# Optimization experiments

Measured on AMD Instinct MI355X. Metric: run time of the kernel, lower is better.

## Reference

```python
import jax, jax.numpy as jnp
import numpy as np

B, T, D = 4, 2048, 1024
H, DH = 16, 64

def setup_inputs() -> dict:
    key = jax.random.key(0)
    k1, k2, k3 = jax.random.split(key, 3)
    x = jax.random.normal(k1, (B, T, D), dtype=jnp.float32)
    ln_gamma = jnp.ones((D,), dtype=jnp.float32)
    ln_beta = jnp.zeros((D,), dtype=jnp.float32)
    W_qkv = jax.random.normal(k2, (3 * D, D), dtype=jnp.float32) * (1.0 / np.sqrt(D))
    W_o = jax.random.normal(k3, (D, D), dtype=jnp.float32) * (1.0 / np.sqrt(D))
    return {"x": x, "ln_gamma": ln_gamma, "ln_beta": ln_beta, "W_qkv": W_qkv, "W_o": W_o}

def reference(x, ln_gamma, ln_beta, W_qkv, W_o):
    b, t, d = x.shape
    scale = 1.0 / np.sqrt(DH)
    # pre-LN in fp32 (eps=1e-5, elementwise affine)
    xf = x.astype(jnp.float32)
    mu = jnp.mean(xf, axis=-1, keepdims=True)
    var = jnp.mean(jnp.square(xf - mu), axis=-1, keepdims=True)
    xn = (xf - mu) * jax.lax.rsqrt(var + 1e-5) * ln_gamma + ln_beta
    xn = xn.astype(x.dtype)
    # fused QKV projection (torch Linear: y = x @ W^T), view as (B,T,H,3*DH)
    qkv = jnp.einsum('btd,ed->bte', xn, W_qkv).reshape(b, t, H, 3 * DH)
    Q, K, V = jnp.split(qkv, 3, axis=-1)  # each (B,T,H,DH)
    # scores (B,H,T,T), causal mask, softmax
    scores = jnp.einsum('bqhd,bkhd->bhqk', Q, K) * scale
    causal = jnp.tril(jnp.ones((t, t), dtype=bool))
    scores = jnp.where(causal, scores, -jnp.inf)
    A = jax.nn.softmax(scores, axis=-1)
    ctx = jnp.einsum('bhqk,bkhd->bqhd', A, V).reshape(b, t, d)
    return jnp.einsum('btd,ed->bte', ctx, W_o)
```

## Files before the change

kernel.cpp:

```cpp
#include <hip/hip_runtime.h>


typedef __attribute__((ext_vector_type(8))) short bf8v;
typedef __attribute__((ext_vector_type(4))) float f4v;

#define Tt  2048
#define Dd  1024
#define Hh  16
#define DHh 64

#if __has_builtin(__builtin_amdgcn_exp2f)
#define EXP2(x) __builtin_amdgcn_exp2f(x)
#else
#define EXP2(x) __expf((x) * 0.69314718056f)
#endif

__device__ __forceinline__ ushort f2bf(float f) {
  union { float f; unsigned v; } c; c.f = f;
  unsigned r = c.v + 0x7fffu + ((c.v >> 16) & 1u);
  return (ushort)(r >> 16);
}
__device__ __forceinline__ ushort f2bf_rn(float f) {
  union { float f; unsigned v; } c; c.f = f;
  return (ushort)((c.v + 0x8000u) >> 16);
}
__device__ __forceinline__ f4v zero4() { f4v z; z[0]=z[1]=z[2]=z[3]=0.f; return z; }

__device__ __forceinline__ void gl_lds16(const ushort* g, ushort* l) {
  __builtin_amdgcn_global_load_lds(
      (const __attribute__((address_space(1))) unsigned*)g,
      (__attribute__((address_space(3))) unsigned*)l, 16, 0, 0);
}

__global__ __launch_bounds__(256)
void prep_k(const float* __restrict__ wqkv, ushort* __restrict__ wqkb,
            const float* __restrict__ wo,   ushort* __restrict__ wob,
            const float* __restrict__ x, const float* __restrict__ g,
            const float* __restrict__ bta, ushort* __restrict__ xn) {
  const int bid = blockIdx.x, tid = threadIdx.x;
  if (bid < 4096) {
    const float4* src = (bid < 3072) ? (const float4*)wqkv : (const float4*)wo;
    ushort4* dst      = (bid < 3072) ? (ushort4*)wqkb : (ushort4*)wob;
    const int i = ((bid < 3072) ? bid : (bid - 3072)) * 256 + tid;
    const float4 v = src[i];
    ushort4 o;
    o.x = f2bf(v.x); o.y = f2bf(v.y); o.z = f2bf(v.z); o.w = f2bf(v.w);
    dst[i] = o;
    return;
  }
  const int row = bid - 4096;
  const float4 v = ((const float4*)(x + row * Dd))[tid];
  float s  = v.x + v.y + v.z + v.w;
  float sq = v.x*v.x + v.y*v.y + v.z*v.z + v.w*v.w;
  #pragma unroll
  for (int off = 32; off; off >>= 1) {
    s  += __shfl_down(s,  off, 64);
    sq += __shfl_down(sq, off, 64);
  }
  __shared__ float red[8];
  const int w = tid >> 6, l = tid & 63;
  if (l == 0) { red[w] = s; red[w + 4] = sq; }
  __syncthreads();
  s  = red[0] + red[1] + red[2] + red[3];
  sq = red[4] + red[5] + red[6] + red[7];
  const float mu  = s * (1.0f / Dd);
  const float var = sq * (1.0f / Dd) - mu * mu;
  const float rs  = rsqrtf(var + 1e-5f);
  const float4 gv = ((const float4*)g)[tid];
  const float4 bv = ((const float4*)bta)[tid];
  ushort4 o;
  o.x = f2bf((v.x - mu) * rs * gv.x + bv.x);
  o.y = f2bf((v.y - mu) * rs * gv.y + bv.y);
  o.z = f2bf((v.z - mu) * rs * gv.z + bv.z);
  o.w = f2bf((v.w - mu) * rs * gv.w + bv.w);
  ((ushort4*)(xn + row * Dd))[tid] = o;
}

template<int MODE>
__global__ __launch_bounds__(256)
void gemm128(const ushort* __restrict__ A, const ushort* __restrict__ Bt,
             void* __restrict__ O0v, ushort* __restrict__ O1, ushort* __restrict__ O2,
             int Kd, int nbm) {
  __shared__ ushort As[2][128 * 64], Bs[2][128 * 64];
  const int tid = threadIdx.x;
  const int l = tid & 63, w = tid >> 6, fr = l & 15, fq = l >> 4;
  const int wm = w & 1, wn = w >> 1;
  const int bm = blockIdx.x % nbm, bn = blockIdx.x / nbm;
  const int gr8 = l >> 3, gc8s = ((l & 7) ^ gr8) * 8;
  const int sw = fr & 7;
  const int cA = (fq ^ sw) * 8, cB = ((4 + fq) ^ sw) * 8;
  const int NIT = Kd >> 6;

  f4v acc[4][4];
  #pragma unroll
  for (int m = 0; m < 4; m++)
    #pragma unroll
    for (int n = 0; n < 4; n++) acc[m][n] = zero4();

  auto stage = [&](int it, int bi) {
    const int k0 = it * 64;
    #pragma unroll
    for (int i = 0; i < 4; i++) {
      const int row = w * 32 + i * 8;
      gl_lds16(A  + (bm * 128 + row + gr8) * Kd + k0 + gc8s, &As[bi][row * 64]);
      gl_lds16(Bt + (bn * 128 + row + gr8) * Kd + k0 + gc8s, &Bs[bi][row * 64]);
    }
  };

  stage(0, 0);
  for (int it = 0; it < NIT; ++it) {
    __syncthreads();
    if (it + 1 < NIT) stage(it + 1, (it + 1) & 1);
    const ushort* Ab = As[it & 1];
    const ushort* Bb = Bs[it & 1];
    #pragma unroll
    for (int kk = 0; kk < 2; kk++) {
      const int cs = kk ? cB : cA;
      bf8v af[4], bf[4];
      #pragma unroll
      for (int m = 0; m < 4; m++)
        af[m] = *(const bf8v*)&Ab[(wm * 64 + m * 16 + fr) * 64 + cs];
      #pragma unroll
      for (int n = 0; n < 4; n++)
        bf[n] = *(const bf8v*)&Bb[(wn * 64 + n * 16 + fr) * 64 + cs];
      #pragma unroll
      for (int m = 0; m < 4; m++)
        #pragma unroll
        for (int n = 0; n < 4; n++)
          acc[m][n] = __builtin_amdgcn_mfma_f32_16x16x32_bf16(af[m], bf[n], acc[m][n], 0, 0, 0);
    }
  }

  #pragma unroll
  for (int m = 0; m < 4; m++) {
    const int grow = bm * 128 + wm * 64 + m * 16 + fq * 4;
    #pragma unroll
    for (int n = 0; n < 4; n++) {
      const int e = bn * 128 + wn * 64 + n * 16 + fr;
      #pragma unroll
      for (int r = 0; r < 4; r++) {
        const int row = grow + r;
        if (MODE == 0) {
          const int h = e / 192, inner = e % 192;
          const int sel = inner >> 6, dh = inner & 63;
          const int bb = row >> 11, t = row & 2047;
          float v = acc[m][n][r];
          if (sel == 0) v *= 0.18033688f;
          ushort* dst = (sel == 0) ? (ushort*)O0v : (sel == 1) ? O1 : O2;
          dst[((bb * Hh + h) * Tt + t) * DHh + dh] = f2bf(v);
        } else {
          ((float*)O0v)[row * Dd + e] = acc[m][n][r];
        }
      }
    }
  }
}

__global__ __launch_bounds__(256)
void vtr_k(const ushort* __restrict__ Vb, ushort* __restrict__ Vtg) {
  __shared__ ushort tile[64 * 72];
  const int tid = threadIdx.x;
  const int tt = blockIdx.x & 31;
  const int hb = blockIdx.x >> 5;
  const int base = hb * Tt * DHh;
  const int srow = tid >> 3, soff = (tid & 7) * 8;
  #pragma unroll
  for (int i = 0; i < 2; i++) {
    const int t = srow + i * 32;
    const uint4 vv = *(const uint4*)(Vb + base + (tt * 64 + t) * DHh + soff);
    const ushort* e = (const ushort*)&vv;
    #pragma unroll
    for (int j = 0; j < 8; j++) tile[(soff + j) * 72 + t] = e[j];
  }
  __syncthreads();
  #pragma unroll
  for (int i = 0; i < 2; i++) {
    const int dh = srow + i * 32;
    *(uint4*)(Vtg + base + dh * Tt + tt * 64 + soff) = *(const uint4*)&tile[dh * 72 + soff];
  }
}

__global__ __launch_bounds__(512)
void attn_k(const ushort* __restrict__ Qb, const ushort* __restrict__ Kb,
            const ushort* __restrict__ Vtg, ushort* __restrict__ ctx) {
  __shared__ ushort QS[128 * 64];
  __shared__ ushort Pb[128 * 68];
  __shared__ ushort Ks[2][64 * 64], Vt[2][64 * 64];
  const int tid = threadIdx.x;
  const int l = tid & 63, w = tid >> 6, fr = l & 15, fq = l >> 4;
  const int bid = blockIdx.x;
  const int hb = (bid & 7) * 8 + (bid >> 6);
  const int u  = (bid >> 3) & 7;
  const int h  = hb & 15, b = hb >> 4;
  const int headbase = hb * Tt * DHh;
  const int gr8 = l >> 3, gc8s = ((l & 7) ^ gr8) * 8;
  const int sw = fr & 7;
  const int cA = (fq ^ sw) * 8, cB = ((4 + fq) ^ sw) * 8;

  auto stageKV = [&](int kt, int bi) {
    const int row = w * 8;
    gl_lds16(Kb  + headbase + (kt * 64 + row + gr8) * DHh + gc8s, &Ks[bi][row * 64]);
    gl_lds16(Vtg + headbase + (row + gr8) * Tt + kt * 64 + gc8s, &Vt[bi][row * 64]);
  };

  for (int half = 0; half < 2; ++half) {
    const int qt = half ? (15 - u) : u;
    const int qrow0w = qt * 128 + w * 16;

    if (half) __syncthreads();

    #pragma unroll
    for (int i = 0; i < 2; i++) {
      const int row = w * 16 + i * 8;
      gl_lds16(Qb + headbase + (qt * 128 + row + gr8) * DHh + gc8s, &QS[row * 64]);
    }
    stageKV(0, 0);
    __syncthreads();

    bf8v aq[2];
    aq[0] = *(const bf8v*)&QS[(w * 16 + fr) * 64 + cA];
    aq[1] = *(const bf8v*)&QS[(w * 16 + fr) * 64 + cB];
    __asm__ __volatile__("" ::: "memory");

    f4v o[4];
    #pragma unroll
    for (int n = 0; n < 4; n++) o[n] = zero4();
    float lsum = 0.f;

    const int ktmax = 2 * qt + 1;
    for (int kt = 0; kt <= ktmax; ++kt) {
      if (kt) __syncthreads();
      if (kt < ktmax) stageKV(kt + 1, (kt + 1) & 1);
      const ushort* K_ = Ks[kt & 1];
      const ushort* V_ = Vt[kt & 1];

      if (kt * 64 <= qrow0w + 15) {
        f4v scT[4];
        #pragma unroll
        for (int n = 0; n < 4; n++) scT[n] = zero4();
        __builtin_amdgcn_s_setprio(1);
        #pragma unroll
        for (int nt = 0; nt < 4; nt++) {
          const bf8v k0 = *(const bf8v*)&K_[(nt * 16 + fr) * 64 + cA];
          const bf8v k1 = *(const bf8v*)&K_[(nt * 16 + fr) * 64 + cB];
          scT[nt] = __builtin_amdgcn_mfma_f32_16x16x32_bf16(k0, aq[0], scT[nt], 0, 0, 0);
          scT[nt] = __builtin_amdgcn_mfma_f32_16x16x32_bf16(k1, aq[1], scT[nt], 0, 0, 0);
        }
        __builtin_amdgcn_s_setprio(0);

        if (kt * 64 + 63 > qrow0w) {
          const int q0 = qrow0w + fr;
          #pragma unroll
          for (int nt = 0; nt < 4; nt++) {
            const int kc0 = kt * 64 + nt * 16 + fq * 4;
            #pragma unroll
            for (int r = 0; r < 4; r++)
              if (kc0 + r > q0) scT[nt][r] = -1e30f;
          }
        }

        {
          const int prow = w * 16 + fr;
          ushort* pbase = &Pb[prow * 68 + fq * 4];
          #pragma unroll
          for (int nt = 0; nt < 4; nt++) {
            const float p0 = EXP2(scT[nt][0]), p1 = EXP2(scT[nt][1]);
            const float p2 = EXP2(scT[nt][2]), p3 = EXP2(scT[nt][3]);
            ushort4 pk;
            pk.x = f2bf_rn(p0); pk.y = f2bf_rn(p1);
            pk.z = f2bf_rn(p2); pk.w = f2bf_rn(p3);
            *(ushort4*)(pbase + nt * 16) = pk;
            lsum += (p0 + p1) + (p2 + p3);
          }
        }

        __asm__ __volatile__("" ::: "memory");

        __builtin_amdgcn_s_setprio(1);
        #pragma unroll
        for (int s = 0; s < 2; s++) {
          const bf8v ap = *(const bf8v*)&Pb[(w * 16 + fr) * 68 + s * 32 + fq * 8];
          #pragma unroll
          for (int nt = 0; nt < 4; nt++) {
            const bf8v bv2 = *(const bf8v*)&V_[(nt * 16 + fr) * 64 + (s ? cB : cA)];
            o[nt] = __builtin_amdgcn_mfma_f32_16x16x32_bf16(ap, bv2, o[nt], 0, 0, 0);
          }
        }
        __builtin_amdgcn_s_setprio(0);
      }
    }

    float t = lsum;
    t += __shfl_xor(t, 16, 64);
    t += __shfl_xor(t, 32, 64);
    const float inv = 1.0f / t;
    #pragma unroll
    for (int r = 0; r < 4; r++) {
      const float iv = __shfl(inv, 20 * fq + r, 64);
      const int rowg = b * Tt + qt * 128 + w * 16 + fq * 4 + r;
      #pragma unroll
      for (int nt = 0; nt < 4; nt++)
        ctx[rowg * Dd + h * DHh + nt * 16 + fr] = f2bf(o[nt][r] * iv);
    }
  }
}

extern "C" void kernel_launch(void* const* d_in, const int* in_sizes, int n_in,
                              void* d_out, int out_size, void* d_ws, size_t ws_size,
                              hipStream_t stream) {
  const float* x    = (const float*)d_in[0];
  const float* g    = (const float*)d_in[1];
  const float* bta  = (const float*)d_in[2];
  const float* wqkv = (const float*)d_in[3];
  const float* wo   = (const float*)d_in[4];

  const int NROW = 4 * Tt;
  const int NQ   = 4 * Hh * Tt * DHh;
  ushort* xn   = (ushort*)d_ws;
  ushort* Qb   = xn + NROW * Dd;
  ushort* Kb   = Qb + NQ;
  ushort* Vb   = Kb + NQ;
  ushort* ctx  = Vb + NQ;
  ushort* wqkb = ctx + NROW * Dd;
  ushort* wob  = wqkb + 3 * Dd * Dd;
  ushort* VbT  = xn;

  prep_k<<<3072 + 1024 + NROW, 256, 0, stream>>>(wqkv, wqkb, wo, wob, x, g, bta, xn);
  gemm128<0><<<64 * 24, 256, 0, stream>>>(xn, wqkb, Qb, Kb, Vb, Dd, 64);
  vtr_k<<<4 * Hh * (Tt / 64), 256, 0, stream>>>(Vb, VbT);
  attn_k<<<4 * Hh * (Tt / 128) / 2, 512, 0, stream>>>(Qb, Kb, VbT, ctx);
  gemm128<1><<<64 * 8, 256, 0, stream>>>(ctx, wob, (void*)d_out, nullptr, nullptr, Dd, 64);
}
```

Measured before the change: 238.3 us.

## Replace QKV projection GEMM with 256x256-tile, 8-wave pipelined kernel

Adds a new QKV projection kernel that computes 256x256 output tiles with 512 threads instead of 128x128 tiles with 256 threads. Each wave computes a 128x64 sub-tile. The K loop is split into four quarter phases that interleave LDS fragment reads, async global-to-LDS staging of the next A and B halves, and MFMA bursts raised with s_setprio. The goal is more data reuse per byte loaded and less global and LDS traffic per FLOP. In exchange it uses about 128KB of LDS per block, which likely allows only one block per CU, and launches only 384 blocks, which risks poor occupancy and an uneven last wave across CUs.

```diff
diff --git a/kernel.cpp b/kernel.cpp
--- a/kernel.cpp
+++ b/kernel.cpp
@@ -76,6 +76,169 @@
   ((ushort4*)(xn + row * Dd))[tid] = o;
 }
 
+__global__ __launch_bounds__(512, 2)
+void gemm256q(const ushort* __restrict__ A, const ushort* __restrict__ Bt,
+              ushort* __restrict__ Oq, ushort* __restrict__ Ok,
+              ushort* __restrict__ Ov, int Kd, int nbm) {
+  __shared__ ushort As[2][2][128 * 64];
+  __shared__ ushort Bs[2][2][128 * 64];
+  const int tid = threadIdx.x;
+  const int l = tid & 63, w = tid >> 6, fr = l & 15, fq = l >> 4;
+  const int wm = w & 1, wn = w >> 1;
+  const int bm = blockIdx.x % nbm, bn = blockIdx.x / nbm;
+  const int gr8 = l >> 3, gc8s = ((l & 7) ^ gr8) * 8;
+  const int sw = fr & 7;
+  const int cA = (fq ^ sw) * 8, cB = ((4 + fq) ^ sw) * 8;
+  const int NIT = Kd >> 6;
+
+  f4v acc[8][4];
+  #pragma unroll
+  for (int m = 0; m < 8; m++)
+    #pragma unroll
+    for (int n = 0; n < 4; n++) acc[m][n] = zero4();
+
+  auto stageA = [&](int t, int half) {
+    const int k0 = t * 64;
+    ushort* dst = &As[t & 1][half][0];
+    const int r0 = bm * 256 + half * 128;
+    #pragma unroll
+    for (int i = 0; i < 2; i++) {
+      const int r = i * 64 + w * 8;
+      gl_lds16(A + (r0 + r + gr8) * Kd + k0 + gc8s, dst + r * 64);
+    }
+  };
+  auto stageB = [&](int t, int half) {
+    const int k0 = t * 64;
+    ushort* dst = &Bs[t & 1][half][0];
+    const int r0 = bn * 256 + half * 128;
+    #pragma unroll
+    for (int i = 0; i < 2; i++) {
+      const int r = i * 64 + w * 8;
+      gl_lds16(Bt + (r0 + r + gr8) * Kd + k0 + gc8s, dst + r * 64);
+    }
+  };
+
+  stageA(0, 0); stageA(0, 1); stageB(0, 0); stageB(0, 1);
+  stageA(1, 0); stageA(1, 1);
+  asm volatile("s_waitcnt vmcnt(4)" ::: "memory");
+  __builtin_amdgcn_sched_barrier(0);
+  __builtin_amdgcn_s_barrier();
+  __builtin_amdgcn_sched_barrier(0);
+
+  for (int t = 0; t < NIT; ++t) {
+    const ushort* Ab = &As[t & 1][wm][0];
+    const ushort* Bb = &Bs[t & 1][wn >> 1][(wn & 1) * (64 * 64)];
+    bf8v a0[4][2], a1[4][2], b0[2][2], b1[2][2];
+
+    #pragma unroll
+    for (int mi = 0; mi < 4; mi++) {
+      a0[mi][0] = *(const bf8v*)&Ab[(mi * 16 + fr) * 64 + cA];
+      a0[mi][1] = *(const bf8v*)&Ab[(mi * 16 + fr) * 64 + cB];
+    }
+    #pragma unroll
+    for (int ni = 0; ni < 2; ni++) {
+      b0[ni][0] = *(const bf8v*)&Bb[(ni * 16 + fr) * 64 + cA];
+      b0[ni][1] = *(const bf8v*)&Bb[(ni * 16 + fr) * 64 + cB];
+    }
+    if (t + 1 < NIT) stageB(t + 1, 0);
+    __builtin_amdgcn_s_barrier();
+    asm volatile("s_waitcnt lgkmcnt(0)" ::: "memory");
+    __builtin_amdgcn_sched_barrier(0);
+    __builtin_amdgcn_s_setprio(1);
+    #pragma unroll
+    for (int mi = 0; mi < 4; mi++)
+      #pragma unroll
+      for (int ni = 0; ni < 2; ni++) {
+        acc[mi][ni] = __builtin_amdgcn_mfma_f32_16x16x32_bf16(a0[mi][0], b0[ni][0], acc[mi][ni], 0, 0, 0);
+        acc[mi][ni] = __builtin_amdgcn_mfma_f32_16x16x32_bf16(a0[mi][1], b0[ni][1], acc[mi][ni], 0, 0, 0);
+      }
+    __builtin_amdgcn_s_setprio(0);
+    __builtin_amdgcn_s_barrier();
+
+    #pragma unroll
+    for (int mi = 0; mi < 4; mi++) {
+      a1[mi][0] = *(const bf8v*)&Ab[((4 + mi) * 16 + fr) * 64 + cA];
+      a1[mi][1] = *(const bf8v*)&Ab[((4 + mi) * 16 + fr) * 64 + cB];
+    }
+    #pragma unroll
+    for (int ni = 0; ni < 2; ni++) {
+      b1[ni][0] = *(const bf8v*)&Bb[((2 + ni) * 16 + fr) * 64 + cA];
+      b1[ni][1] = *(const bf8v*)&Bb[((2 + ni) * 16 + fr) * 64 + cB];
+    }
+    if (t + 1 < NIT) stageB(t + 1, 1);
+    __builtin_amdgcn_s_barrier();
+    asm volatile("s_waitcnt lgkmcnt(0)" ::: "memory");
+    __builtin_amdgcn_sched_barrier(0);
+    __builtin_amdgcn_s_setprio(1);
+    #pragma unroll
+    for (int mi = 0; mi < 4; mi++)
+      #pragma unroll
+      for (int ni = 0; ni < 2; ni++) {
+        acc[mi][2 + ni] = __builtin_amdgcn_mfma_f32_16x16x32_bf16(a0[mi][0], b1[ni][0], acc[mi][2 + ni], 0, 0, 0);
+        acc[mi][2 + ni] = __builtin_amdgcn_mfma_f32_16x16x32_bf16(a0[mi][1], b1[ni][1], acc[mi][2 + ni], 0, 0, 0);
+      }
+    __builtin_amdgcn_s_setprio(0);
+    __builtin_amdgcn_s_barrier();
+
+    #pragma unroll
+    for (int ni = 0; ni < 2; ni++) {
+      b0[ni][0] = *(const bf8v*)&Bb[(ni * 16 + fr) * 64 + cA];
+      b0[ni][1] = *(const bf8v*)&Bb[(ni * 16 + fr) * 64 + cB];
+    }
+    if (t + 2 < NIT) stageA(t + 2, 0);
+    __builtin_amdgcn_s_barrier();
+    asm volatile("s_waitcnt lgkmcnt(0)" ::: "memory");
+    __builtin_amdgcn_sched_barrier(0);
+    __builtin_amdgcn_s_setprio(1);
+    #pragma unroll
+    for (int mi = 0; mi < 4; mi++)
+      #pragma unroll
+      for (int ni = 0; ni < 2; ni++) {
+        acc[4 + mi][ni] = __builtin_amdgcn_mfma_f32_16x16x32_bf16(a1[mi][0], b0[ni][0], acc[4 + mi][ni], 0, 0, 0);
+        acc[4 + mi][ni] = __builtin_amdgcn_mfma_f32_16x16x32_bf16(a1[mi][1], b0[ni][1], acc[4 + mi][ni], 0, 0, 0);
+      }
+    __builtin_amdgcn_s_setprio(0);
+    __builtin_amdgcn_s_barrier();
+
+    if (t + 2 < NIT) stageA(t + 2, 1);
+    __builtin_amdgcn_s_barrier();
+    __builtin_amdgcn_s_setprio(1);
+    #pragma unroll
+    for (int mi = 0; mi < 4; mi++)
+      #pragma unroll
+      for (int ni = 0; ni < 2; ni++) {
+        acc[4 + mi][2 + ni] = __builtin_amdgcn_mfma_f32_16x16x32_bf16(a1[mi][0], b1[ni][0], acc[4 + mi][2 + ni], 0, 0, 0);
+        acc[4 + mi][2 + ni] = __builtin_amdgcn_mfma_f32_16x16x32_bf16(a1[mi][1], b1[ni][1], acc[4 + mi][2 + ni], 0, 0, 0);
+      }
+    __builtin_amdgcn_s_setprio(0);
+    if (t + 2 < NIT) asm volatile("s_waitcnt vmcnt(4)" ::: "memory");
+    else             asm volatile("s_waitcnt vmcnt(0)" ::: "memory");
+    __builtin_amdgcn_sched_barrier(0);
+    __builtin_amdgcn_s_barrier();
+    __builtin_amdgcn_sched_barrier(0);
+  }
+
+  #pragma unroll
+  for (int mi = 0; mi < 8; mi++) {
+    const int grow = bm * 256 + wm * 128 + mi * 16 + fq * 4;
+    #pragma unroll
+    for (int ni = 0; ni < 4; ni++) {
+      const int e = bn * 256 + wn * 64 + ni * 16 + fr;
+      const int h = e / 192, inner = e % 192;
+      const int sel = inner >> 6, dh = inner & 63;
+      ushort* dst = (sel == 0) ? Oq : (sel == 1) ? Ok : Ov;
+      #pragma unroll
+      for (int r = 0; r < 4; r++) {
+        const int row = grow + r;
+        const int bb = row >> 11, tt = row & 2047;
+        float v = acc[mi][ni][r];
+        if (sel == 0) v *= 0.18033688f;
+        dst[((bb * Hh + h) * Tt + tt) * DHh + dh] = f2bf(v);
+      }
+    }
+  }
+}
+
 template<int MODE>
 __global__ __launch_bounds__(256)
 void gemm128(const ushort* __restrict__ A, const ushort* __restrict__ Bt,
@@ -326,7 +489,7 @@
   ushort* VbT  = xn;
 
   prep_k<<<3072 + 1024 + NROW, 256, 0, stream>>>(wqkv, wqkb, wo, wob, x, g, bta, xn);
-  gemm128<0><<<64 * 24, 256, 0, stream>>>(xn, wqkb, Qb, Kb, Vb, Dd, 64);
+  gemm256q<<<32 * 12, 512, 0, stream>>>(xn, wqkb, Qb, Kb, Vb, Dd, 32);
   vtr_k<<<4 * Hh * (Tt / 64), 256, 0, stream>>>(Vb, VbT);
   attn_k<<<4 * Hh * (Tt / 128) / 2, 512, 0, stream>>>(Qb, Kb, VbT, ctx);
   gemm128<1><<<64 * 8, 256, 0, stream>>>(ctx, wob, (void*)d_out, nullptr, nullptr, Dd, 64);
```

Result: slower. 245.0 us (+2.8%).

## Fuse V transpose into QKV GEMM epilogue via LDS staging

Applied to the files above, without the earlier changes.

Removes the separate V-transpose kernel. The QKV GEMM epilogue now stages the V tile in shared memory and writes it directly in transposed (dh, t) layout, and attention reads it from there. This saves one kernel launch plus a full global round-trip of V, at the cost of extra syncthreads and LDS traffic in the GEMM epilogue. It relies on the As buffer being large enough for a 64x140 tile.

```diff
diff --git a/kernel.cpp b/kernel.cpp
--- a/kernel.cpp
+++ b/kernel.cpp
@@ -143,10 +143,11 @@
         if (MODE == 0) {
           const int h = e / 192, inner = e % 192;
           const int sel = inner >> 6, dh = inner & 63;
+          if (sel == 2) continue;
           const int bb = row >> 11, t = row & 2047;
           float v = acc[m][n][r];
           if (sel == 0) v *= 0.18033688f;
-          ushort* dst = (sel == 0) ? (ushort*)O0v : (sel == 1) ? O1 : O2;
+          ushort* dst = (sel == 0) ? (ushort*)O0v : O1;
           dst[((bb * Hh + h) * Tt + t) * DHh + dh] = f2bf(v);
         } else {
           ((float*)O0v)[row * Dd + e] = acc[m][n][r];
@@ -154,29 +155,44 @@
       }
     }
   }
-}
-
-__global__ __launch_bounds__(256)
-void vtr_k(const ushort* __restrict__ Vb, ushort* __restrict__ Vtg) {
-  __shared__ ushort tile[64 * 72];
-  const int tid = threadIdx.x;
-  const int tt = blockIdx.x & 31;
-  const int hb = blockIdx.x >> 5;
-  const int base = hb * Tt * DHh;
-  const int srow = tid >> 3, soff = (tid & 7) * 8;
-  #pragma unroll
-  for (int i = 0; i < 2; i++) {
-    const int t = srow + i * 32;
-    const uint4 vv = *(const uint4*)(Vb + base + (tt * 64 + t) * DHh + soff);
-    const ushort* e = (const ushort*)&vv;
-    #pragma unroll
-    for (int j = 0; j < 8; j++) tile[(soff + j) * 72 + t] = e[j];
-  }
-  __syncthreads();
-  #pragma unroll
-  for (int i = 0; i < 2; i++) {
-    const int dh = srow + i * 32;
-    *(uint4*)(Vtg + base + dh * Tt + tt * 64 + soff) = *(const uint4*)&tile[dh * 72 + soff];
+
+  if (MODE == 0) {
+    const int bnm3 = bn % 3;
+    if (bnm3 != 0) {
+      const int vrun = (bnm3 == 1) ? 0 : 1;
+      ushort* Vl = &As[0][0];
+      __syncthreads();
+      if (wn == vrun) {
+        #pragma unroll
+        for (int m = 0; m < 4; m++) {
+          const int row0 = wm * 64 + m * 16 + fq * 4;
+          #pragma unroll
+          for (int n = 0; n < 4; n++) {
+            const int col = n * 16 + fr;
+            ushort4 pk;
+            pk.x = f2bf(acc[m][n][0]); pk.y = f2bf(acc[m][n][1]);
+            pk.z = f2bf(acc[m][n][2]); pk.w = f2bf(acc[m][n][3]);
+            *(ushort4*)&Vl[col * 140 + row0] = pk;
+          }
+        }
+      }
+      __syncthreads();
+      const int evr = bn * 128 + vrun * 64;
+      const int hq  = evr / 192;
+      const int bb  = bm >> 4, t0g = (bm & 15) * 128;
+      ushort* vdst = O2 + (bb * Hh + hq) * (size_t)(DHh * Tt) + t0g;
+      #pragma unroll
+      for (int i = 0; i < 4; i++) {
+        const int u = i * 256 + tid;
+        const int dh = u >> 4, tc = (u & 15) * 8;
+        const ushort4 lo = *(const ushort4*)&Vl[dh * 140 + tc];
+        const ushort4 hi = *(const ushort4*)&Vl[dh * 140 + tc + 4];
+        union { ushort s[8]; uint4 v; } pk;
+        pk.s[0] = lo.x; pk.s[1] = lo.y; pk.s[2] = lo.z; pk.s[3] = lo.w;
+        pk.s[4] = hi.x; pk.s[5] = hi.y; pk.s[6] = hi.z; pk.s[7] = hi.w;
+        *(uint4*)&vdst[dh * Tt + tc] = pk.v;
+      }
+    }
   }
 }
 
@@ -323,11 +339,9 @@
   ushort* ctx  = Vb + NQ;
   ushort* wqkb = ctx + NROW * Dd;
   ushort* wob  = wqkb + 3 * Dd * Dd;
-  ushort* VbT  = xn;
 
   prep_k<<<3072 + 1024 + NROW, 256, 0, stream>>>(wqkv, wqkb, wo, wob, x, g, bta, xn);
   gemm128<0><<<64 * 24, 256, 0, stream>>>(xn, wqkb, Qb, Kb, Vb, Dd, 64);
-  vtr_k<<<4 * Hh * (Tt / 64), 256, 0, stream>>>(Vb, VbT);
-  attn_k<<<4 * Hh * (Tt / 128) / 2, 512, 0, stream>>>(Qb, Kb, VbT, ctx);
+  attn_k<<<4 * Hh * (Tt / 128) / 2, 512, 0, stream>>>(Qb, Kb, Vb, ctx);
   gemm128<1><<<64 * 8, 256, 0, stream>>>(ctx, wob, (void*)d_out, nullptr, nullptr, Dd, 64);
 }
```

New measurement: 231.3 us. 1.03x faster.
